# Kernel optimization log

Hardware: AMD Instinct MI355X
Metric: run time of the kernel (lower is better)

Reference implementation:

```python
import jax, jax.numpy as jnp
import numpy as np

FREQ_DIM = 64
BLOCK_DIM = 64
N = 256          # lattice sites
CH = 6           # channel_num -> block diagonals at offsets -1, 0, +1
S = 2 * 16 + CH - 2   # seq_num = 36
BS = 4           # block_size (kron of two 2x2 matrices)
HID = 128
EPS = 1e-5
B = 32

_e = np.eye(2)
_sx = np.array([[0., 1.], [1., 0.]])
_siy = np.array([[0., 1.], [-1., 0.]])
_sz = np.array([[1., 0.], [0., -1.]])
_p = [_e, _sx, _siy, _sz]
KRONS = jnp.asarray(np.stack([np.kron(_p[a], _p[b]) for a in range(4) for b in range(4)]).astype(np.float32))  # (16,4,4)
Z1 = KRONS[12]  # kron(sigma_z, I) used for interaction blocks ('z1')


def _bn(h, g, b):
    # BatchNorm1d in training mode: biased batch statistics over axis 0
    mu = h.mean(axis=0)
    v = h.var(axis=0)
    return g * (h - mu) / jnp.sqrt(v + EPS) + b


def _mlp(x, Win, bin_, Wmid, bmid, Wout, bout, gamma, beta):
    # depth-4 MLP: Lin+ReLU, then (BN,Lin,ReLU) x2, then BN,Lin,ReLU
    h = jax.nn.relu(x @ Win + bin_)
    for i in range(Wmid.shape[0]):
        h = jax.nn.relu(_bn(h, gamma[i], beta[i]) @ Wmid[i] + bmid[i])
    return jax.nn.relu(_bn(h, gamma[-1], beta[-1]) @ Wout + bout)


def _lstm(xs, h0, c0, Wih, Whh, bih, bhh):
    # xs: (B, T, S); torch gate order i, f, g, o
    def step(carry, x_t):
        h, c = carry
        gates = x_t @ Wih.T + h @ Whh.T + (bih + bhh)
        i, f, g, o = jnp.split(gates, 4, axis=-1)
        c = jax.nn.sigmoid(f) * c + jax.nn.sigmoid(i) * jnp.tanh(g)
        h = jax.nn.sigmoid(o) * jnp.tanh(c)
        return (h, c), h
    _, hs = jax.lax.scan(step, (h0, c0), jnp.swapaxes(xs, 0, 1))
    return jnp.swapaxes(hs, 0, 1)


def setup_inputs() -> dict:
    key = jax.random.key(0)
    ks = iter(jax.random.split(key, 48))
    def w(shape, s=0.05):
        return jax.random.normal(next(ks), shape, dtype=jnp.float32) * s
    d = {
        'x': w((B, FREQ_DIM + BLOCK_DIM), 1.0),
        'fd_Win': w((FREQ_DIM, HID)), 'fd_bin': w((HID,)),
        'fd_Wmid': w((2, HID, HID)), 'fd_bmid': w((2, HID)),
        'fd_Wout': w((HID, S)), 'fd_bout': w((S,)),
        'fd_gamma': jnp.ones((3, HID), jnp.float32), 'fd_beta': jnp.zeros((3, HID), jnp.float32),
        'bd_Win': w((BLOCK_DIM, HID)), 'bd_bin': w((HID,)),
        'bd_Wmid': w((2, HID, HID)), 'bd_bmid': w((2, HID)),
        'bd_Wout': w((HID, S)), 'bd_bout': w((S,)),
        'bd_gamma': jnp.ones((3, HID), jnp.float32), 'bd_beta': jnp.zeros((3, HID), jnp.float32),
        'sc_Win': w((S, 1, HID)), 'sc_bin': w((S, HID)),
        'sc_Wmid': w((S, 2, HID, HID)), 'sc_bmid': w((S, 2, HID)),
        'sc_Wout': w((S, HID, N)), 'sc_bout': w((S, N)),
        'sc_gamma': jnp.ones((S, 3, HID), jnp.float32), 'sc_beta': jnp.zeros((S, 3, HID), jnp.float32),
        'lstm_Wih': w((4 * S, S)), 'lstm_Whh': w((4 * S, S)),
        'lstm_bih': w((4 * S,)), 'lstm_bhh': w((4 * S,)),
        'mix_W': w((S, 2 * S)), 'mix_b': w((S,)),
    }
    return d


def reference(x, fd_Win, fd_bin, fd_Wmid, fd_bmid, fd_Wout, fd_bout, fd_gamma, fd_beta,
              bd_Win, bd_bin, bd_Wmid, bd_bmid, bd_Wout, bd_bout, bd_gamma, bd_beta,
              sc_Win, sc_bin, sc_Wmid, sc_bmid, sc_Wout, sc_bout, sc_gamma, sc_beta,
              lstm_Wih, lstm_Whh, lstm_bih, lstm_bhh, mix_W, mix_b):
    Bsz = x.shape[0]
    block = _mlp(x[:, FREQ_DIM:], bd_Win, bd_bin, bd_Wmid, bd_bmid, bd_Wout, bd_bout, bd_gamma, bd_beta)  # (B,S)
    freq = _mlp(x[:, :FREQ_DIM], fd_Win, fd_bin, fd_Wmid, fd_bmid, fd_Wout, fd_bout, fd_gamma, fd_beta)   # (B,S)
    # S independent scalar->N MLPs, batched with vmap over the stacked params
    sc = jax.vmap(_mlp)(freq.T[:, :, None], sc_Win, sc_bin, sc_Wmid, sc_bmid,
                        sc_Wout, sc_bout, sc_gamma, sc_beta)  # (S,B,N)
    freq_seq = jnp.cos(sc).transpose(1, 2, 0)   # (B,N,S)
    seq = _lstm(freq_seq, block, jnp.zeros_like(block), lstm_Wih, lstm_Whh, lstm_bih, lstm_bhh)  # (B,N,S)
    block_seq = jnp.concatenate([jnp.broadcast_to(block[:, :, None], (Bsz, S, N)),
                                 jnp.swapaxes(seq, 1, 2)], axis=1)  # (B,2S,N)
    # 1x1 Conv2d == channel mixing matmul
    mixed = jnp.einsum('bcn,oc->bon', block_seq, mix_W) + mix_b[None, :, None]  # (B,S,N)
    inter = mixed[:, :CH - 2]                          # (B,CH-2,N)
    onsite = mixed[:, CH - 2:].reshape(Bsz, 2, 16, N)  # (B,2,16,N)
    H_int = jnp.einsum('bcn,ij->bcnij', inter, Z1)         # (B,CH-2,N,4,4)
    H_os = jnp.einsum('bgkn,kij->bgnij', onsite, KRONS)    # (B,2,N,4,4) summed over 16 pairs
    half = (CH - 2) // 2
    strips = jnp.concatenate([H_int[:, :half], H_os, H_int[:, half:]], axis=1)  # (B,CH,N,4,4)
    strips = strips.reshape(Bsz, CH // 2, 2, N, BS, BS)
    # banded block assembly: strip i lives on block-diagonal offset i - (CH//2)//2
    grid = jnp.zeros((Bsz, 2, N, N, BS, BS), dtype=x.dtype)
    for i in range(CH // 2):
        o = i - (CH // 2) // 2
        rows = jnp.arange(N - abs(o)) + max(0, -o)
        cols = rows + o
        grid = grid.at[:, :, rows, cols].set(strips[:, i][:, :, rows])
    matrix = grid.transpose(0, 1, 2, 4, 3, 5).reshape(Bsz, 2, N * BS, N * BS)
    return matrix
```

## Files before the change

kernel.cpp:

```cpp
#include <hip/hip_runtime.h>
#include <math.h>

#define EPSF 1e-5f
typedef __attribute__((ext_vector_type(2))) float f32x2;
typedef __attribute__((ext_vector_type(4))) float f32x4;

__device__ __forceinline__ float pauliv(int p, int r, int c) {
    switch (p) {
        case 0: return (r == c) ? 1.f : 0.f;
        case 1: return (r != c) ? 1.f : 0.f;
        case 2: return (r == 0 && c == 1) ? 1.f : ((r == 1 && c == 0) ? -1.f : 0.f);
        default: return (r == c) ? ((r == 0) ? 1.f : -1.f) : 0.f;
    }
}

__device__ void mlp64_body(const float* __restrict__ xin,
                           const float* __restrict__ Win,
                           const float* __restrict__ bin_,
                           const float* __restrict__ Wmid,
                           const float* __restrict__ bmid,
                           const float* __restrict__ Wout,
                           const float* __restrict__ bout,
                           const float* __restrict__ gamma,
                           const float* __restrict__ beta,
                           float* __restrict__ out)
{
    __shared__ float sX[2048];
    __shared__ float sA[4096];
    __shared__ float sB[4096];
    __shared__ float sMu[128], sRs[128];
    int tid = threadIdx.x;

    for (int idx = tid; idx < 2048; idx += 512) {
        int b = idx >> 6, c = idx & 63;
        sX[idx] = xin[b * 128 + c];
    }
    __syncthreads();

    for (int idx = tid; idx < 4096; idx += 512) {
        int b = idx >> 7, j = idx & 127;
        float acc = bin_[j];
        for (int c = 0; c < 64; ++c) acc = fmaf(sX[b * 64 + c], Win[c * 128 + j], acc);
        sA[idx] = fmaxf(acc, 0.f);
    }
    __syncthreads();

    float* cur = sA;
    float* nxt = sB;
    for (int l = 0; l < 3; ++l) {
        if (tid < 128) {
            float s = 0.f, s2 = 0.f;
            for (int b = 0; b < 32; ++b) {
                float v = cur[b * 128 + tid];
                s += v; s2 += v * v;
            }
            float mu = s * (1.f / 32.f);
            float var = s2 * (1.f / 32.f) - mu * mu;
            sMu[tid] = mu;
            sRs[tid] = rsqrtf(var + EPSF);
        }
        __syncthreads();
        for (int idx = tid; idx < 4096; idx += 512) {
            int j = idx & 127;
            cur[idx] = gamma[l * 128 + j] * (cur[idx] - sMu[j]) * sRs[j] + beta[l * 128 + j];
        }
        __syncthreads();
        if (l < 2) {
            for (int idx = tid; idx < 4096; idx += 512) {
                int b = idx >> 7, j = idx & 127;
                float acc = bmid[l * 128 + j];
                for (int c = 0; c < 128; ++c)
                    acc = fmaf(cur[b * 128 + c], Wmid[(l * 128 + c) * 128 + j], acc);
                nxt[idx] = fmaxf(acc, 0.f);
            }
            __syncthreads();
            float* t = cur; cur = nxt; nxt = t;
        } else {
            for (int idx = tid; idx < 1152; idx += 512) {
                int b = idx / 36, j = idx - b * 36;
                float acc = bout[j];
                for (int c = 0; c < 128; ++c)
                    acc = fmaf(cur[b * 128 + c], Wout[c * 36 + j], acc);
                out[idx] = fmaxf(acc, 0.f);
            }
        }
    }
}

__global__ __launch_bounds__(512) void k_mlp2(
    const float* __restrict__ x,
    const float* fdWin, const float* fdbin, const float* fdWmid, const float* fdbmid,
    const float* fdWout, const float* fdbout, const float* fdg, const float* fdbt,
    const float* bdWin, const float* bdbin, const float* bdWmid, const float* bdbmid,
    const float* bdWout, const float* bdbout, const float* bdg, const float* bdbt,
    float* freq, float* blk)
{
    if (blockIdx.x == 0)
        mlp64_body(x + 64, bdWin, bdbin, bdWmid, bdbmid, bdWout, bdbout, bdg, bdbt, blk);
    else
        mlp64_body(x, fdWin, fdbin, fdWmid, fdbmid, fdWout, fdbout, fdg, fdbt, freq);
}

__global__ __launch_bounds__(512) void k_sc(
    const float* __restrict__ freq,
    const float* __restrict__ Win,
    const float* __restrict__ bin_,
    const float* __restrict__ Wmid,
    const float* __restrict__ bmid,
    const float* __restrict__ Wout,
    const float* __restrict__ bout,
    const float* __restrict__ gamma,
    const float* __restrict__ beta,
    float* __restrict__ fseq2)
{
    int s = blockIdx.x, tid = threadIdx.x;
    __shared__ float sA[4096];
    __shared__ float sB[4096];
    __shared__ float sMu[128], sRs[128];
    const float* Wm = Wmid + (size_t)s * 2 * 128 * 128;
    const float* Wo = Wout + (size_t)s * 128 * 256;
    const float* gm = gamma + s * 3 * 128;
    const float* bt = beta + s * 3 * 128;

    for (int idx = tid; idx < 4096; idx += 512) {
        int b = idx >> 7, j = idx & 127;
        float acc = fmaf(freq[b * 36 + s], Win[s * 128 + j], bin_[s * 128 + j]);
        sA[idx] = fmaxf(acc, 0.f);
    }
    __syncthreads();

    float* cur = sA;
    float* nxt = sB;
    for (int l = 0; l < 3; ++l) {
        if (tid < 128) {
            float sm = 0.f, s2 = 0.f;
            for (int b = 0; b < 32; ++b) {
                float v = cur[b * 128 + tid];
                sm += v; s2 += v * v;
            }
            float mu = sm * (1.f / 32.f);
            float var = s2 * (1.f / 32.f) - mu * mu;
            sMu[tid] = mu;
            sRs[tid] = rsqrtf(var + EPSF);
        }
        __syncthreads();
        for (int idx = tid; idx < 4096; idx += 512) {
            int j = idx & 127;
            cur[idx] = gm[l * 128 + j] * (cur[idx] - sMu[j]) * sRs[j] + bt[l * 128 + j];
        }
        __syncthreads();
        if (l < 2) {
            int jj = tid & 127, bb = tid >> 7;
            float acc[8];
            #pragma unroll
            for (int k = 0; k < 8; ++k) acc[k] = bmid[(s * 2 + l) * 128 + jj];
            for (int c = 0; c < 128; ++c) {
                float w = Wm[(l * 128 + c) * 128 + jj];
                #pragma unroll
                for (int k = 0; k < 8; ++k)
                    acc[k] = fmaf(cur[(bb + 4 * k) * 128 + c], w, acc[k]);
            }
            __syncthreads();
            #pragma unroll
            for (int k = 0; k < 8; ++k) nxt[(bb + 4 * k) * 128 + jj] = fmaxf(acc[k], 0.f);
            __syncthreads();
            float* t = cur; cur = nxt; nxt = t;
        } else {
            int nn = tid & 255, bb2 = tid >> 8;
            float acc[16];
            #pragma unroll
            for (int k = 0; k < 16; ++k) acc[k] = bout[s * 256 + nn];
            for (int c = 0; c < 128; ++c) {
                float w = Wo[c * 256 + nn];
                #pragma unroll
                for (int k = 0; k < 16; ++k)
                    acc[k] = fmaf(cur[(bb2 + 2 * k) * 128 + c], w, acc[k]);
            }
            #pragma unroll
            for (int k = 0; k < 16; ++k) {
                float v = fmaxf(acc[k], 0.f);
                fseq2[((size_t)s * 32 + bb2 + 2 * k) * 256 + nn] = __cosf(v);
            }
        }
    }
}

__global__ __launch_bounds__(512) void k_xg(
    const float* __restrict__ fseq2, const float* __restrict__ Wih,
    const float* __restrict__ bih, const float* __restrict__ bhh,
    float* __restrict__ Xg)
{
    int t = blockIdx.x, tid = threadIdx.x;
    __shared__ float sF[1152];
    __shared__ float sWt[36 * 144];
    for (int idx = tid; idx < 1152; idx += 512) {
        int s = idx >> 5, b = idx & 31;
        sF[b * 36 + s] = fseq2[(size_t)idx * 256 + t];
    }
    for (int idx = tid; idx < 5184; idx += 512) {
        int j = idx / 36, s = idx - j * 36;
        sWt[s * 144 + j] = Wih[idx];
    }
    __syncthreads();
    for (int idx = tid; idx < 4608; idx += 512) {
        int b = idx / 144, j = idx - b * 144;
        int g = j / 36, u = j - g * 36;
        float acc = bih[j] + bhh[j];
        #pragma unroll
        for (int s = 0; s < 36; ++s)
            acc = fmaf(sF[b * 36 + s], sWt[s * 144 + j], acc);
        Xg[(((size_t)b * 256 + t) * 36 + u) * 4 + g] = acc;
    }
}

#define TSTEPS 16
__global__ __launch_bounds__(64, 1) void k_lstm(
    const float* __restrict__ Xg,
    const float* __restrict__ blk,
    const float* __restrict__ Whh,
    float* __restrict__ hseqT)
{
    int b = blockIdx.x;
    int lane = threadIdx.x;
    int uu = lane < 36 ? lane : 35;
    bool active = lane < 36;

    __shared__ float lxg[2][TSTEPS * 144];

    f32x2 wif[36], wgo[36];
    #pragma unroll
    for (int k = 0; k < 36; ++k) {
        wif[k] = f32x2{Whh[uu * 36 + k], Whh[(36 + uu) * 36 + k]};
        wgo[k] = f32x2{Whh[(72 + uu) * 36 + k], Whh[(108 + uu) * 36 + k]};
    }
    float h = blk[b * 36 + uu];
    float c = 0.f;
    const f32x4* xb = (const f32x4*)(Xg + (size_t)b * 256 * 144);
    float* hout = hseqT + ((size_t)b * 36 + uu) * 256;

    f32x4 stg[9];
    #pragma unroll
    for (int i = 0; i < 9; ++i) stg[i] = xb[i * 64 + lane];
    #pragma unroll
    for (int i = 0; i < 9; ++i) ((f32x4*)&lxg[0][0])[i * 64 + lane] = stg[i];

    for (int tt = 0; tt < 256 / TSTEPS; ++tt) {
        const int cur = tt & 1;
        if (tt < 256 / TSTEPS - 1) {
            const f32x4* src = xb + (size_t)(tt + 1) * (TSTEPS * 36);
            #pragma unroll
            for (int i = 0; i < 9; ++i) stg[i] = src[i * 64 + lane];
        }

        #pragma unroll
        for (int s = 0; s < TSTEPS; ++s) {
            f32x4 xg4 = ((const f32x4*)&lxg[cur][s * 144])[uu];
            f32x2 a0 = f32x2{xg4.x, xg4.y};
            f32x2 b0 = f32x2{xg4.z, xg4.w};
            f32x2 a1 = f32x2{0.f, 0.f};
            f32x2 b1 = f32x2{0.f, 0.f};
            #pragma unroll
            for (int k = 0; k < 36; k += 2) {
                float h0 = __int_as_float(__builtin_amdgcn_readlane(__float_as_int(h), k));
                float h1 = __int_as_float(__builtin_amdgcn_readlane(__float_as_int(h), k + 1));
                a0 = __builtin_elementwise_fma(wif[k], f32x2{h0, h0}, a0);
                b0 = __builtin_elementwise_fma(wgo[k], f32x2{h0, h0}, b0);
                a1 = __builtin_elementwise_fma(wif[k + 1], f32x2{h1, h1}, a1);
                b1 = __builtin_elementwise_fma(wgo[k + 1], f32x2{h1, h1}, b1);
            }
            a0 += a1; b0 += b1;
            float iv = 1.f / (1.f + __expf(-a0.x));
            float fv = 1.f / (1.f + __expf(-a0.y));
            float gv = 1.f - 2.f / (__expf(2.f * b0.x) + 1.f);
            float ov = 1.f / (1.f + __expf(-b0.y));
            c = fmaf(fv, c, iv * gv);
            h = ov * (1.f - 2.f / (__expf(2.f * c) + 1.f));
            if (active) hout[tt * TSTEPS + s] = h;
        }

        if (tt < 256 / TSTEPS - 1) {
            #pragma unroll
            for (int i = 0; i < 9; ++i)
                ((f32x4*)&lxg[cur ^ 1][0])[i * 64 + lane] = stg[i];
        }
    }
}

__global__ __launch_bounds__(256) void k_mixed(
    const float* __restrict__ blk, const float* __restrict__ hseqT,
    const float* __restrict__ mixW, const float* __restrict__ mixb,
    float* __restrict__ mixed)
{
    int bq = blockIdx.x;
    int b = bq >> 2, oq = bq & 3;
    int tid = threadIdx.x;
    __shared__ float sH[36 * 256];
    __shared__ float sW[9 * 36];
    __shared__ float sBase[9];
    for (int idx = tid; idx < 9216; idx += 256)
        sH[idx] = hseqT[(size_t)b * 9216 + idx];
    for (int idx = tid; idx < 9 * 36; idx += 256) {
        int o = idx / 36, u = idx - o * 36;
        sW[idx] = mixW[(oq * 9 + o) * 72 + 36 + u];
    }
    if (tid < 9) {
        int o = oq * 9 + tid;
        float acc = mixb[o];
        for (int c = 0; c < 36; ++c) acc = fmaf(mixW[o * 72 + c], blk[b * 36 + c], acc);
        sBase[tid] = acc;
    }
    __syncthreads();
    int n = tid;
    #pragma unroll
    for (int o = 0; o < 9; ++o) {
        float acc = sBase[o];
        #pragma unroll
        for (int u = 0; u < 36; ++u)
            acc = fmaf(sW[o * 36 + u], sH[u * 256 + n], acc);
        mixed[((size_t)b * 36 + oq * 9 + o) * 256 + n] = acc;
    }
}

__global__ __launch_bounds__(256) void k_asm(
    const float* __restrict__ mixed, float* __restrict__ out)
{
    int wg = blockIdx.x;
    int n = wg & 255, bg = wg >> 8;
    int g = bg & 1, b = bg >> 1;
    const float* mb = mixed + (size_t)b * 36 * 256 + n;
    float vSub = mb[(size_t)g * 256];
    float vSup = mb[(size_t)(2 + g) * 256];
    float ch[16];
    #pragma unroll
    for (int k = 0; k < 16; ++k) ch[k] = mb[(size_t)(4 + 16 * g + k) * 256];
    float d[16];
    #pragma unroll
    for (int e = 0; e < 16; ++e) {
        int r = e >> 2, cc = e & 3;
        float acc = 0.f;
        #pragma unroll
        for (int k = 0; k < 16; ++k) {
            float kv = pauliv(k >> 2, r >> 1, cc >> 1) * pauliv(k & 3, r & 1, cc & 1);
            if (kv == 1.f) acc = acc + ch[k];
            else if (kv == -1.f) acc = acc - ch[k];
        }
        d[e] = acc;
    }

    f32x4* outp = (f32x4*)out + ((size_t)bg * 1024 + 4 * n) * 256;
    int m = threadIdx.x;
    if (m == n) {
        #pragma unroll
        for (int r = 0; r < 4; ++r)
            __builtin_nontemporal_store(
                f32x4{d[r * 4 + 0], d[r * 4 + 1], d[r * 4 + 2], d[r * 4 + 3]},
                &outp[r * 256 + m]);
    } else if (m == n - 1) {
        __builtin_nontemporal_store(f32x4{vSub, 0.f, 0.f, 0.f}, &outp[0 * 256 + m]);
        __builtin_nontemporal_store(f32x4{0.f, vSub, 0.f, 0.f}, &outp[1 * 256 + m]);
        __builtin_nontemporal_store(f32x4{0.f, 0.f, -vSub, 0.f}, &outp[2 * 256 + m]);
        __builtin_nontemporal_store(f32x4{0.f, 0.f, 0.f, -vSub}, &outp[3 * 256 + m]);
    } else if (m == n + 1) {
        __builtin_nontemporal_store(f32x4{vSup, 0.f, 0.f, 0.f}, &outp[0 * 256 + m]);
        __builtin_nontemporal_store(f32x4{0.f, vSup, 0.f, 0.f}, &outp[1 * 256 + m]);
        __builtin_nontemporal_store(f32x4{0.f, 0.f, -vSup, 0.f}, &outp[2 * 256 + m]);
        __builtin_nontemporal_store(f32x4{0.f, 0.f, 0.f, -vSup}, &outp[3 * 256 + m]);
    } else {
        f32x4 z = f32x4{0.f, 0.f, 0.f, 0.f};
        #pragma unroll
        for (int r = 0; r < 4; ++r)
            __builtin_nontemporal_store(z, &outp[r * 256 + m]);
    }
}

extern "C" void kernel_launch(void* const* d_in, const int* in_sizes, int n_in,
                              void* d_out, int out_size, void* d_ws, size_t ws_size,
                              hipStream_t stream) {
    const float* x      = (const float*)d_in[0];
    const float* fdWin  = (const float*)d_in[1];
    const float* fdbin  = (const float*)d_in[2];
    const float* fdWmid = (const float*)d_in[3];
    const float* fdbmid = (const float*)d_in[4];
    const float* fdWout = (const float*)d_in[5];
    const float* fdbout = (const float*)d_in[6];
    const float* fdg    = (const float*)d_in[7];
    const float* fdbt   = (const float*)d_in[8];
    const float* bdWin  = (const float*)d_in[9];
    const float* bdbin  = (const float*)d_in[10];
    const float* bdWmid = (const float*)d_in[11];
    const float* bdbmid = (const float*)d_in[12];
    const float* bdWout = (const float*)d_in[13];
    const float* bdbout = (const float*)d_in[14];
    const float* bdg    = (const float*)d_in[15];
    const float* bdbt   = (const float*)d_in[16];
    const float* scWin  = (const float*)d_in[17];
    const float* scbin  = (const float*)d_in[18];
    const float* scWmid = (const float*)d_in[19];
    const float* scbmid = (const float*)d_in[20];
    const float* scWout = (const float*)d_in[21];
    const float* scbout = (const float*)d_in[22];
    const float* scg    = (const float*)d_in[23];
    const float* scbt   = (const float*)d_in[24];
    const float* Wih    = (const float*)d_in[25];
    const float* Whh    = (const float*)d_in[26];
    const float* bih    = (const float*)d_in[27];
    const float* bhh    = (const float*)d_in[28];
    const float* mixW   = (const float*)d_in[29];
    const float* mixb   = (const float*)d_in[30];

    float* ws    = (float*)d_ws;
    float* freq  = ws;
    float* blk   = ws + 1152;
    float* fseq2 = ws + 2304;
    float* Xg    = ws + 297216;
    float* hseqT = ws + 1476864;
    float* mixed = ws + 1771776;

    k_mlp2<<<2, 512, 0, stream>>>(x,
        fdWin, fdbin, fdWmid, fdbmid, fdWout, fdbout, fdg, fdbt,
        bdWin, bdbin, bdWmid, bdbmid, bdWout, bdbout, bdg, bdbt,
        freq, blk);
    k_sc<<<36, 512, 0, stream>>>(freq, scWin, scbin, scWmid, scbmid,
                                 scWout, scbout, scg, scbt, fseq2);
    k_xg<<<256, 512, 0, stream>>>(fseq2, Wih, bih, bhh, Xg);
    k_lstm<<<32, 64, 0, stream>>>(Xg, blk, Whh, hseqT);
    k_mixed<<<128, 256, 0, stream>>>(blk, hseqT, mixW, mixb, mixed);
    k_asm<<<16384, 256, 0, stream>>>(mixed, (float*)d_out);
}
```

Baseline: 333.9 us.

## Split output into zero-fill plus sparse band writes; parallelize sc output layer

Replaces the per-element assembly kernel with a bulk vectorized zero fill of the output followed by a small kernel that writes only the diagonal and off-diagonal band entries. Splits the sc MLP's final layer into a separate kernel over 144 blocks, staging activations through workspace. This aims to cut branchy per-block assembly work and raise parallelism in the output projection, at the cost of extra launches and a global round trip for the activations.

```diff
diff --git a/kernel.cpp b/kernel.cpp
--- a/kernel.cpp
+++ b/kernel.cpp
@@ -101,24 +101,21 @@
         mlp64_body(x, fdWin, fdbin, fdWmid, fdbmid, fdWout, fdbout, fdg, fdbt, freq);
 }
 
-__global__ __launch_bounds__(512) void k_sc(
+__global__ __launch_bounds__(512) void k_sc1(
     const float* __restrict__ freq,
     const float* __restrict__ Win,
     const float* __restrict__ bin_,
     const float* __restrict__ Wmid,
     const float* __restrict__ bmid,
-    const float* __restrict__ Wout,
-    const float* __restrict__ bout,
     const float* __restrict__ gamma,
     const float* __restrict__ beta,
-    float* __restrict__ fseq2)
+    float* __restrict__ actW)
 {
     int s = blockIdx.x, tid = threadIdx.x;
     __shared__ float sA[4096];
     __shared__ float sB[4096];
     __shared__ float sMu[128], sRs[128];
     const float* Wm = Wmid + (size_t)s * 2 * 128 * 128;
-    const float* Wo = Wout + (size_t)s * 128 * 256;
     const float* gm = gamma + s * 3 * 128;
     const float* bt = beta + s * 3 * 128;
 
@@ -166,22 +163,43 @@
             __syncthreads();
             float* t = cur; cur = nxt; nxt = t;
         } else {
-            int nn = tid & 255, bb2 = tid >> 8;
-            float acc[16];
-            #pragma unroll
-            for (int k = 0; k < 16; ++k) acc[k] = bout[s * 256 + nn];
-            for (int c = 0; c < 128; ++c) {
-                float w = Wo[c * 256 + nn];
-                #pragma unroll
-                for (int k = 0; k < 16; ++k)
-                    acc[k] = fmaf(cur[(bb2 + 2 * k) * 128 + c], w, acc[k]);
-            }
-            #pragma unroll
-            for (int k = 0; k < 16; ++k) {
-                float v = fmaxf(acc[k], 0.f);
-                fseq2[((size_t)s * 32 + bb2 + 2 * k) * 256 + nn] = __cosf(v);
-            }
-        }
+            for (int idx = tid; idx < 4096; idx += 512)
+                actW[(size_t)s * 4096 + idx] = cur[idx];
+        }
+    }
+}
+
+__global__ __launch_bounds__(512) void k_sc2(
+    const float* __restrict__ actW,
+    const float* __restrict__ Wout,
+    const float* __restrict__ bout,
+    float* __restrict__ fseq2)
+{
+    int bidx = blockIdx.x;
+    int s = bidx >> 2, q = bidx & 3;
+    int tid = threadIdx.x;
+    __shared__ float sAct[4096];
+    for (int idx = tid; idx < 4096; idx += 512)
+        sAct[idx] = actW[(size_t)s * 4096 + idx];
+    __syncthreads();
+
+    int nn = (tid & 63) + q * 64;
+    int bb = tid >> 6;
+    const float* Wo = Wout + (size_t)s * 128 * 256;
+    float acc[4];
+    #pragma unroll
+    for (int k = 0; k < 4; ++k) acc[k] = bout[s * 256 + nn];
+    #pragma unroll 4
+    for (int c = 0; c < 128; ++c) {
+        float w = Wo[c * 256 + nn];
+        #pragma unroll
+        for (int k = 0; k < 4; ++k)
+            acc[k] = fmaf(sAct[(bb + 8 * k) * 128 + c], w, acc[k]);
+    }
+    #pragma unroll
+    for (int k = 0; k < 4; ++k) {
+        float v = fmaxf(acc[k], 0.f);
+        fseq2[((size_t)s * 32 + bb + 8 * k) * 256 + nn] = __cosf(v);
     }
 }
 
@@ -321,18 +339,27 @@
     }
 }
 
-__global__ __launch_bounds__(256) void k_asm(
+__global__ __launch_bounds__(256) void k_zero(float* __restrict__ out, long total4)
+{
+    f32x4* o = (f32x4*)out;
+    f32x4 z = f32x4{0.f, 0.f, 0.f, 0.f};
+    long stride = (long)gridDim.x * 256;
+    for (long i = (long)blockIdx.x * 256 + threadIdx.x; i < total4; i += stride)
+        o[i] = z;
+}
+
+__global__ __launch_bounds__(256) void k_sparse(
     const float* __restrict__ mixed, float* __restrict__ out)
 {
-    int wg = blockIdx.x;
-    int n = wg & 255, bg = wg >> 8;
+    int bg = blockIdx.x;
     int g = bg & 1, b = bg >> 1;
-    const float* mb = mixed + (size_t)b * 36 * 256 + n;
-    float vSub = mb[(size_t)g * 256];
-    float vSup = mb[(size_t)(2 + g) * 256];
+    int n = threadIdx.x;
+    const float* mb = mixed + (size_t)b * 36 * 256;
+    float vSub = mb[(size_t)g * 256 + n];
+    float vSup = mb[(size_t)(2 + g) * 256 + n];
     float ch[16];
     #pragma unroll
-    for (int k = 0; k < 16; ++k) ch[k] = mb[(size_t)(4 + 16 * g + k) * 256];
+    for (int k = 0; k < 16; ++k) ch[k] = mb[(size_t)(4 + 16 * g + k) * 256 + n];
     float d[16];
     #pragma unroll
     for (int e = 0; e < 16; ++e) {
@@ -347,29 +374,20 @@
         d[e] = acc;
     }
 
-    f32x4* outp = (f32x4*)out + ((size_t)bg * 1024 + 4 * n) * 256;
-    int m = threadIdx.x;
-    if (m == n) {
+    float* base = out + (size_t)bg * 1024 * 1024;
+    #pragma unroll
+    for (int r = 0; r < 4; ++r)
+        *(f32x4*)(base + (size_t)(4 * n + r) * 1024 + 4 * n) =
+            f32x4{d[r * 4 + 0], d[r * 4 + 1], d[r * 4 + 2], d[r * 4 + 3]};
+    if (n > 0) {
         #pragma unroll
         for (int r = 0; r < 4; ++r)
-            __builtin_nontemporal_store(
-                f32x4{d[r * 4 + 0], d[r * 4 + 1], d[r * 4 + 2], d[r * 4 + 3]},
-                &outp[r * 256 + m]);
-    } else if (m == n - 1) {
-        __builtin_nontemporal_store(f32x4{vSub, 0.f, 0.f, 0.f}, &outp[0 * 256 + m]);
-        __builtin_nontemporal_store(f32x4{0.f, vSub, 0.f, 0.f}, &outp[1 * 256 + m]);
-        __builtin_nontemporal_store(f32x4{0.f, 0.f, -vSub, 0.f}, &outp[2 * 256 + m]);
-        __builtin_nontemporal_store(f32x4{0.f, 0.f, 0.f, -vSub}, &outp[3 * 256 + m]);
-    } else if (m == n + 1) {
-        __builtin_nontemporal_store(f32x4{vSup, 0.f, 0.f, 0.f}, &outp[0 * 256 + m]);
-        __builtin_nontemporal_store(f32x4{0.f, vSup, 0.f, 0.f}, &outp[1 * 256 + m]);
-        __builtin_nontemporal_store(f32x4{0.f, 0.f, -vSup, 0.f}, &outp[2 * 256 + m]);
-        __builtin_nontemporal_store(f32x4{0.f, 0.f, 0.f, -vSup}, &outp[3 * 256 + m]);
-    } else {
-        f32x4 z = f32x4{0.f, 0.f, 0.f, 0.f};
+            base[(size_t)(4 * n + r) * 1024 + 4 * (n - 1) + r] = (r < 2) ? vSub : -vSub;
+    }
+    if (n < 255) {
         #pragma unroll
         for (int r = 0; r < 4; ++r)
-            __builtin_nontemporal_store(z, &outp[r * 256 + m]);
+            base[(size_t)(4 * n + r) * 1024 + 4 * (n + 1) + r] = (r < 2) ? vSup : -vSup;
     }
 }
 
@@ -415,15 +433,20 @@
     float* Xg    = ws + 297216;
     float* hseqT = ws + 1476864;
     float* mixed = ws + 1771776;
-
+    float* actW  = Xg;
+
+    float* out = (float*)d_out;
+    long total4 = (long)out_size / 4;
+
+    k_zero<<<2048, 256, 0, stream>>>(out, total4);
     k_mlp2<<<2, 512, 0, stream>>>(x,
         fdWin, fdbin, fdWmid, fdbmid, fdWout, fdbout, fdg, fdbt,
         bdWin, bdbin, bdWmid, bdbmid, bdWout, bdbout, bdg, bdbt,
         freq, blk);
-    k_sc<<<36, 512, 0, stream>>>(freq, scWin, scbin, scWmid, scbmid,
-                                 scWout, scbout, scg, scbt, fseq2);
+    k_sc1<<<36, 512, 0, stream>>>(freq, scWin, scbin, scWmid, scbmid, scg, scbt, actW);
+    k_sc2<<<144, 512, 0, stream>>>(actW, scWout, scbout, fseq2);
     k_xg<<<256, 512, 0, stream>>>(fseq2, Wih, bih, bhh, Xg);
     k_lstm<<<32, 64, 0, stream>>>(Xg, blk, Whh, hseqT);
     k_mixed<<<128, 256, 0, stream>>>(blk, hseqT, mixW, mixb, mixed);
-    k_asm<<<16384, 256, 0, stream>>>(mixed, (float*)d_out);
-}
+    k_sparse<<<64, 256, 0, stream>>>(mixed, out);
+}
```

Measured after the change: 315.1 us. -5.6%, faster.
